# Optimization experiments

Measured on AMD Instinct MI355X. Metric: run time of the kernel, lower is better.

The kernel has to match this reference:

```python
import jax, jax.numpy as jnp
import numpy as np

NEG_SLOPE = 0.01  # torch F.leaky_relu_ default


def setup_inputs() -> dict:
    key = jax.random.key(0)
    k1, k2, k3, k4, k5 = jax.random.split(key, 5)
    N, Fin, Fout = 8192, 256, 128
    X = jax.random.normal(k1, (N, Fin), dtype=jnp.float32)
    adj = jax.random.randint(k2, (N, N), 0, 2, dtype=jnp.int32)
    W = jax.random.normal(k3, (Fout, Fin), dtype=jnp.float32) * 0.05
    b = jax.random.normal(k4, (Fout,), dtype=jnp.float32) * 0.05
    S = jax.random.normal(k5, (2 * Fout,), dtype=jnp.float32)
    return {"X": X, "adj": adj, "W": W, "b": b, "S": S}


def reference(X, adj, W, b, S):
    # X' = W X + b  -> (N, Fout)
    Xp = X @ W.T + b
    N, Fout = Xp.shape
    S_src, S_dst = S[:Fout], S[Fout:]
    # e_ij = leaky_relu(S . [x'_i ; x'_j]) = leaky_relu(S_src.x'_i + S_dst.x'_j)
    e = jax.nn.leaky_relu(
        (Xp @ S_src)[:, None] + (Xp @ S_dst)[None, :], NEG_SLOPE
    )  # (N, N)
    # neighbor set = nonzero entries of adj row plus self-loop
    mask = (adj != 0) | jnp.eye(N, dtype=bool)
    e = jnp.where(mask, e, -jnp.inf)
    attn = jax.nn.softmax(e, axis=1)  # segment softmax over each row's neighbors
    out = jax.nn.sigmoid(attn @ Xp)  # (N, Fout)
    return out
```

## Files before the change

kernel.cpp:

```cpp
#include <hip/hip_runtime.h>

typedef unsigned short u16;
typedef __attribute__((ext_vector_type(8))) u16 u16x8;
typedef __attribute__((ext_vector_type(8))) __bf16 bf16x8;
typedef __attribute__((ext_vector_type(4))) float f32x4;
typedef __attribute__((ext_vector_type(4))) int i32x4;

#define NN 8192
#define FIN 256
#define FOUT 128
#define PW 512
#define NP (NN / PW)
#define WSTRIDE 520

__device__ __forceinline__ u16 f2bf(float f) {
  unsigned u = __float_as_uint(f);
  u += 0x7fffu + ((u >> 16) & 1u);
  return (u16)(u >> 16);
}
__device__ __forceinline__ u16 f2bft(float f) {
  return (u16)(__float_as_uint(f) >> 16);
}
__device__ __forceinline__ float bf2f(u16 s) {
  return __uint_as_float(((unsigned)s) << 16);
}
__device__ __forceinline__ i32x4 ntload4(const int* p) {
  return __builtin_nontemporal_load((const i32x4*)p);
}

__global__ __launch_bounds__(256) void k_splitw(const float* __restrict__ W,
                                                u16* __restrict__ Whi,
                                                u16* __restrict__ Wlo) {
  int t = blockIdx.x * 256 + threadIdx.x;
  float w = W[t];
  u16 hi = f2bf(w);
  Whi[t] = hi;
  Wlo[t] = f2bf(w - bf2f(hi));
}

__global__ __launch_bounds__(256) void k_xp(const float* __restrict__ X,
    const u16* __restrict__ Whi, const u16* __restrict__ Wlo,
    const float* __restrict__ bias, const float* __restrict__ S,
    const int* __restrict__ adj,
    u16* __restrict__ Bsw, float* __restrict__ cexpA,
    u16* __restrict__ jebA, u16* __restrict__ jeb2A, float* __restrict__ diagW) {
  __shared__ float Xs[16 * 260];
  __shared__ float Xp[16 * 132];
  __shared__ float Ss[256];
  const int tid = threadIdx.x;
  const int i0 = blockIdx.x * 16;
  Ss[tid] = S[tid];
  {
    int r = tid >> 4, c = (tid & 15) * 16;
    const float* src = X + (size_t)(i0 + r) * FIN + c;
    float* dst = Xs + r * 260 + c;
#pragma unroll
    for (int k = 0; k < 16; k += 4) *(float4*)(dst + k) = *(const float4*)(src + k);
  }
  __syncthreads();

  const int w = tid >> 6, l = tid & 63, li = l & 15, quad = l >> 4;
  f32x4 acc[2];
  acc[0] = f32x4{0.f, 0.f, 0.f, 0.f};
  acc[1] = f32x4{0.f, 0.f, 0.f, 0.f};
  for (int k0 = 0; k0 < FIN; k0 += 32) {
    const float* xp = Xs + li * 260 + k0 + quad * 8;
    float4 xa = *(const float4*)xp;
    float4 xb = *(const float4*)(xp + 4);
    float xv[8] = {xa.x, xa.y, xa.z, xa.w, xb.x, xb.y, xb.z, xb.w};
    u16x8 ahiu, alou;
#pragma unroll
    for (int jj = 0; jj < 8; ++jj) {
      u16 h = f2bf(xv[jj]);
      ahiu[jj] = h;
      alou[jj] = f2bf(xv[jj] - bf2f(h));
    }
    bf16x8 ahi = __builtin_bit_cast(bf16x8, ahiu);
    bf16x8 alo = __builtin_bit_cast(bf16x8, alou);
#pragma unroll
    for (int t2 = 0; t2 < 2; ++t2) {
      int f = (w * 2 + t2) * 16 + li;
      size_t wofs = (size_t)f * FIN + k0 + quad * 8;
      bf16x8 bhi = __builtin_bit_cast(bf16x8, *(const u16x8*)(Whi + wofs));
      bf16x8 blo = __builtin_bit_cast(bf16x8, *(const u16x8*)(Wlo + wofs));
      acc[t2] = __builtin_amdgcn_mfma_f32_16x16x32_bf16(ahi, bhi, acc[t2], 0, 0, 0);
      acc[t2] = __builtin_amdgcn_mfma_f32_16x16x32_bf16(alo, bhi, acc[t2], 0, 0, 0);
      acc[t2] = __builtin_amdgcn_mfma_f32_16x16x32_bf16(ahi, blo, acc[t2], 0, 0, 0);
    }
  }
#pragma unroll
  for (int t2 = 0; t2 < 2; ++t2) {
    int f = (w * 2 + t2) * 16 + li;
    float bv = bias[f];
#pragma unroll
    for (int r = 0; r < 4; ++r)
      Xp[(quad * 4 + r) * 132 + f] = acc[t2][r] + bv;
  }
  __syncthreads();

  {
    int li2 = tid & 15, q2sub = (tid >> 4) & 1, nt = tid >> 5;
    int f = nt * 16 + li2;
    int rb = q2sub * 8;
    int q2 = ((i0 & 16) >> 3) + q2sub;
    u16x8 ou;
#pragma unroll
    for (int jj = 0; jj < 8; ++jj) ou[jj] = f2bf(Xp[(rb + jj) * 132 + f]);
    *(u16x8*)(Bsw + ((size_t)(i0 >> 5) * 8 + nt) * 512 + (size_t)(q2 * 16 + li2) * 8) = ou;
  }

  {
    int r = tid >> 4, sub = tid & 15;
    float pa = 0.f, pb = 0.f;
#pragma unroll
    for (int m = 0; m < 8; ++m) {
      float x = Xp[r * 132 + sub + m * 16];
      pa += x * Ss[sub + m * 16];
      pb += x * Ss[128 + sub + m * 16];
    }
    pa += __shfl_xor(pa, 1); pa += __shfl_xor(pa, 2);
    pa += __shfl_xor(pa, 4); pa += __shfl_xor(pa, 8);
    pb += __shfl_xor(pb, 1); pb += __shfl_xor(pb, 2);
    pb += __shfl_xor(pb, 4); pb += __shfl_xor(pb, 8);
    if (sub == 0) {
      int i = i0 + r;
      float cc = expf(-0.99f * pa);
      u16 ebq = f2bf(expf(pb));
      u16 e2q = f2bf(expf(0.01f * pb));
      cexpA[i] = cc;
      jebA[i] = ebq;
      jeb2A[i] = e2q;
      float wii = fmaxf(bf2f(ebq), cc * bf2f(e2q));
      float wq = bf2f(f2bft(wii));
      int ad = adj[(size_t)i * NN + i];
      diagW[i] = (ad != 0) ? 0.f : wq;
    }
  }
}

__global__ __launch_bounds__(512, 4) void k_gat(const int* __restrict__ adj,
    const u16* __restrict__ Bsw, const float* __restrict__ cexpA,
    const u16* __restrict__ jebA, const u16* __restrict__ jeb2A,
    const float* __restrict__ diagW, float* __restrict__ out) {
  __shared__ u16 wb[2][16 * WSTRIDE];
  __shared__ float sacc[16 * 132];
  __shared__ float sden[16];
  const int tid = threadIdx.x;
  const int i0 = blockIdx.x * 16;
  const int w = tid >> 6, l = tid & 63, li = l & 15, quad = l >> 4;

  {
    int r = tid >> 5, f = (tid & 31) * 4;
    int i = i0 + r;
    float dw = diagW[i];
    size_t slotbase = (size_t)(i0 >> 5) * 8;
    int laneq = ((i & 31) >> 3) * 16;
    int elem = i & 7;
    float4 v;
    float* vp = &v.x;
#pragma unroll
    for (int k = 0; k < 4; ++k) {
      int ff = f + k;
      u16 xb = Bsw[(slotbase + (ff >> 4)) * 512 + (size_t)(laneq + (ff & 15)) * 8 + elem];
      vp[k] = dw * bf2f(xb);
    }
    *(float4*)&sacc[r * 132 + f] = v;
    if (tid < 16) sden[tid] = diagW[i0 + tid];
  }

  const int r0 = 2 * w;
  const float c0 = cexpA[i0 + r0];
  const float c1 = cexpA[i0 + r0 + 1];
  const int* arow0 = adj + (size_t)(i0 + r0) * NN;
  const int* arow1 = arow0 + NN;

  i32x4 pa[4];
  ushort4 teb[2], te2[2];

  auto stage_load = [&](int p) {
    int base = p * PW + l * 4;
#pragma unroll
    for (int k = 0; k < 2; ++k) {
      pa[k * 2]     = ntload4(arow0 + base + k * 256);
      pa[k * 2 + 1] = ntload4(arow1 + base + k * 256);
      teb[k] = *(const ushort4*)(jebA + base + k * 256);
      te2[k] = *(const ushort4*)(jeb2A + base + k * 256);
    }
  };

  auto stage_store = [&](int buf) {
#pragma unroll
    for (int r2 = 0; r2 < 2; ++r2) {
      float cr = r2 ? c1 : c0;
#pragma unroll
      for (int k = 0; k < 2; ++k) {
        const i32x4 av = pa[k * 2 + r2];
        const u16* ebp = (const u16*)&teb[k];
        const u16* e2p = (const u16*)&te2[k];
        float wv[4];
#pragma unroll
        for (int e = 0; e < 4; ++e) {
          float ww = fmaxf(bf2f(ebp[e]), cr * bf2f(e2p[e]));
          wv[e] = (av[e] != 0) ? ww : 0.f;
        }
        unsigned p0 = __builtin_amdgcn_perm(__float_as_uint(wv[1]),
                                            __float_as_uint(wv[0]), 0x07060302u);
        unsigned p1 = __builtin_amdgcn_perm(__float_as_uint(wv[3]),
                                            __float_as_uint(wv[2]), 0x07060302u);
        *(uint2*)&wb[buf][(r0 + r2) * WSTRIDE + k * 256 + l * 4] = make_uint2(p0, p1);
      }
    }
  };

  f32x4 acc[8];
#pragma unroll
  for (int nt = 0; nt < 8; ++nt) acc[nt] = f32x4{0.f, 0.f, 0.f, 0.f};
  f32x4 accD = f32x4{0.f, 0.f, 0.f, 0.f};
  u16x8 onesu;
#pragma unroll
  for (int jj = 0; jj < 8; ++jj) onesu[jj] = 0x3F80;
  const bf16x8 ONES = __builtin_bit_cast(bf16x8, onesu);

  auto compute = [&](int p, int buf) {
#pragma unroll
    for (int t = 0; t < 2; ++t) {
      int s = w * 2 + t;
      u16x8 au = *(const u16x8*)&wb[buf][li * WSTRIDE + s * 32 + quad * 8];
      bf16x8 A = __builtin_bit_cast(bf16x8, au);
      const u16* bb = Bsw + (size_t)(p * 16 + s) * 4096 + (size_t)l * 8;
#pragma unroll
      for (int nt = 0; nt < 8; ++nt) {
        bf16x8 B = __builtin_bit_cast(bf16x8, *(const u16x8*)(bb + nt * 512));
        acc[nt] = __builtin_amdgcn_mfma_f32_16x16x32_bf16(A, B, acc[nt], 0, 0, 0);
      }
      accD = __builtin_amdgcn_mfma_f32_16x16x32_bf16(A, ONES, accD, 0, 0, 0);
    }
  };

  stage_load(0);
  stage_store(0);
  __syncthreads();
  for (int p = 0; p < NP; ++p) {
    if (p + 1 < NP) stage_load(p + 1);
    compute(p, p & 1);
    if (p + 1 < NP) stage_store((p + 1) & 1);
    __syncthreads();
  }

  if (li == 0) {
#pragma unroll
    for (int r = 0; r < 4; ++r) atomicAdd(&sden[quad * 4 + r], accD[r]);
  }
#pragma unroll
  for (int nt = 0; nt < 8; ++nt) {
#pragma unroll
    for (int r = 0; r < 4; ++r)
      atomicAdd(&sacc[(quad * 4 + r) * 132 + nt * 16 + li], acc[nt][r]);
  }
  __syncthreads();

  {
    int r = tid >> 5, c4 = (tid & 31) * 4;
    float4 v = *(const float4*)&sacc[r * 132 + c4];
    float rd = 1.f / sden[r];
    float o[4] = {v.x, v.y, v.z, v.w};
#pragma unroll
    for (int k = 0; k < 4; ++k) {
      float t = o[k] * rd;
      o[k] = 1.f / (1.f + __expf(-t));
    }
    *(float4*)(out + (size_t)(i0 + r) * FOUT + c4) = make_float4(o[0], o[1], o[2], o[3]);
  }
}

extern "C" void kernel_launch(void* const* d_in, const int* in_sizes, int n_in,
                              void* d_out, int out_size, void* d_ws, size_t ws_size,
                              hipStream_t stream) {
  const float* X = (const float*)d_in[0];
  const int* adj = (const int*)d_in[1];
  const float* W = (const float*)d_in[2];
  const float* bias = (const float*)d_in[3];
  const float* S = (const float*)d_in[4];
  float* out = (float*)d_out;

  char* ws = (char*)d_ws;
  u16* Bsw      = (u16*)(ws);
  u16* Whi      = (u16*)(ws + 2097152);
  u16* Wlo      = (u16*)(ws + 2162688);
  float* cexpA  = (float*)(ws + 2228224);
  u16* jebA     = (u16*)(ws + 2260992);
  u16* jeb2A    = (u16*)(ws + 2277376);
  float* diagW  = (float*)(ws + 2293760);

  hipLaunchKernelGGL(k_splitw, dim3(128), dim3(256), 0, stream, W, Whi, Wlo);
  hipLaunchKernelGGL(k_xp, dim3(512), dim3(256), 0, stream, X, Whi, Wlo, bias, S, adj,
                     Bsw, cexpA, jebA, jeb2A, diagW);
  hipLaunchKernelGGL(k_gat, dim3(512), dim3(512), 0, stream, adj, Bsw, cexpA,
                     jebA, jeb2A, diagW, out);
}
```

Baseline: 440.5 us.

## Split GAT column range across two blocks with global atomic partial sums

```diff
diff --git a/kernel.cpp b/kernel.cpp
--- a/kernel.cpp
+++ b/kernel.cpp
@@ -10,7 +10,7 @@
 #define FIN 256
 #define FOUT 128
 #define PW 512
-#define NP (NN / PW)
+#define NPB 8
 #define WSTRIDE 520
 
 __device__ __forceinline__ u16 f2bf(float f) {
@@ -23,6 +23,9 @@
 }
 __device__ __forceinline__ float bf2f(u16 s) {
   return __uint_as_float(((unsigned)s) << 16);
+}
+__device__ __forceinline__ float trunc_bf(float f) {
+  return __uint_as_float(__float_as_uint(f) & 0xffff0000u);
 }
 __device__ __forceinline__ i32x4 ntload4(const int* p) {
   return __builtin_nontemporal_load((const i32x4*)p);
@@ -43,10 +46,12 @@
     const float* __restrict__ bias, const float* __restrict__ S,
     const int* __restrict__ adj,
     u16* __restrict__ Bsw, float* __restrict__ cexpA,
-    u16* __restrict__ jebA, u16* __restrict__ jeb2A, float* __restrict__ diagW) {
+    u16* __restrict__ jebA, u16* __restrict__ jeb2A,
+    float* __restrict__ pnum, float* __restrict__ pden) {
   __shared__ float Xs[16 * 260];
   __shared__ float Xp[16 * 132];
   __shared__ float Ss[256];
+  __shared__ float ds_dw[16];
   const int tid = threadIdx.x;
   const int i0 = blockIdx.x * 16;
   Ss[tid] = S[tid];
@@ -133,40 +138,36 @@
       float wii = fmaxf(bf2f(ebq), cc * bf2f(e2q));
       float wq = bf2f(f2bft(wii));
       int ad = adj[(size_t)i * NN + i];
-      diagW[i] = (ad != 0) ? 0.f : wq;
-    }
-  }
-}
-
-__global__ __launch_bounds__(512, 4) void k_gat(const int* __restrict__ adj,
+      ds_dw[r] = (ad != 0) ? 0.f : wq;
+    }
+  }
+  __syncthreads();
+
+  {
+    int r = tid >> 4, f8 = (tid & 15) * 8;
+    int i = i0 + r;
+    float dw = ds_dw[r];
+    float o[8];
+#pragma unroll
+    for (int k = 0; k < 8; ++k)
+      o[k] = dw * bf2f(f2bf(Xp[r * 132 + f8 + k]));
+    float* np = pnum + (size_t)i * FOUT + f8;
+    *(float4*)np = make_float4(o[0], o[1], o[2], o[3]);
+    *(float4*)(np + 4) = make_float4(o[4], o[5], o[6], o[7]);
+    if ((tid & 15) == 0) pden[i] = dw;
+  }
+}
+
+__global__ __launch_bounds__(512, 8) void k_gat(const int* __restrict__ adj,
     const u16* __restrict__ Bsw, const float* __restrict__ cexpA,
     const u16* __restrict__ jebA, const u16* __restrict__ jeb2A,
-    const float* __restrict__ diagW, float* __restrict__ out) {
+    float* __restrict__ pnum, float* __restrict__ pden) {
   __shared__ u16 wb[2][16 * WSTRIDE];
-  __shared__ float sacc[16 * 132];
-  __shared__ float sden[16];
   const int tid = threadIdx.x;
-  const int i0 = blockIdx.x * 16;
+  const int rt = blockIdx.x >> 1, ch = blockIdx.x & 1;
+  const int i0 = rt * 16;
+  const int colbase = ch * 4096;
   const int w = tid >> 6, l = tid & 63, li = l & 15, quad = l >> 4;
-
-  {
-    int r = tid >> 5, f = (tid & 31) * 4;
-    int i = i0 + r;
-    float dw = diagW[i];
-    size_t slotbase = (size_t)(i0 >> 5) * 8;
-    int laneq = ((i & 31) >> 3) * 16;
-    int elem = i & 7;
-    float4 v;
-    float* vp = &v.x;
-#pragma unroll
-    for (int k = 0; k < 4; ++k) {
-      int ff = f + k;
-      u16 xb = Bsw[(slotbase + (ff >> 4)) * 512 + (size_t)(laneq + (ff & 15)) * 8 + elem];
-      vp[k] = dw * bf2f(xb);
-    }
-    *(float4*)&sacc[r * 132 + f] = v;
-    if (tid < 16) sden[tid] = diagW[i0 + tid];
-  }
 
   const int r0 = 2 * w;
   const float c0 = cexpA[i0 + r0];
@@ -176,9 +177,10 @@
 
   i32x4 pa[4];
   ushort4 teb[2], te2[2];
+  float dpart0 = 0.f, dpart1 = 0.f;
 
   auto stage_load = [&](int p) {
-    int base = p * PW + l * 4;
+    int base = colbase + p * PW + l * 4;
 #pragma unroll
     for (int k = 0; k < 2; ++k) {
       pa[k * 2]     = ntload4(arow0 + base + k * 256);
@@ -192,6 +194,7 @@
 #pragma unroll
     for (int r2 = 0; r2 < 2; ++r2) {
       float cr = r2 ? c1 : c0;
+      float dsum = 0.f;
 #pragma unroll
       for (int k = 0; k < 2; ++k) {
         const i32x4 av = pa[k * 2 + r2];
@@ -202,6 +205,7 @@
         for (int e = 0; e < 4; ++e) {
           float ww = fmaxf(bf2f(ebp[e]), cr * bf2f(e2p[e]));
           wv[e] = (av[e] != 0) ? ww : 0.f;
+          dsum += trunc_bf(wv[e]);
         }
         unsigned p0 = __builtin_amdgcn_perm(__float_as_uint(wv[1]),
                                             __float_as_uint(wv[0]), 0x07060302u);
@@ -209,17 +213,13 @@
                                             __float_as_uint(wv[2]), 0x07060302u);
         *(uint2*)&wb[buf][(r0 + r2) * WSTRIDE + k * 256 + l * 4] = make_uint2(p0, p1);
       }
+      if (r2) dpart1 += dsum; else dpart0 += dsum;
     }
   };
 
   f32x4 acc[8];
 #pragma unroll
   for (int nt = 0; nt < 8; ++nt) acc[nt] = f32x4{0.f, 0.f, 0.f, 0.f};
-  f32x4 accD = f32x4{0.f, 0.f, 0.f, 0.f};
-  u16x8 onesu;
-#pragma unroll
-  for (int jj = 0; jj < 8; ++jj) onesu[jj] = 0x3F80;
-  const bf16x8 ONES = __builtin_bit_cast(bf16x8, onesu);
 
   auto compute = [&](int p, int buf) {
 #pragma unroll
@@ -227,50 +227,57 @@
       int s = w * 2 + t;
       u16x8 au = *(const u16x8*)&wb[buf][li * WSTRIDE + s * 32 + quad * 8];
       bf16x8 A = __builtin_bit_cast(bf16x8, au);
-      const u16* bb = Bsw + (size_t)(p * 16 + s) * 4096 + (size_t)l * 8;
+      const u16* bb = Bsw + (size_t)(ch * 128 + p * 16 + s) * 4096 + (size_t)l * 8;
 #pragma unroll
       for (int nt = 0; nt < 8; ++nt) {
         bf16x8 B = __builtin_bit_cast(bf16x8, *(const u16x8*)(bb + nt * 512));
         acc[nt] = __builtin_amdgcn_mfma_f32_16x16x32_bf16(A, B, acc[nt], 0, 0, 0);
       }
-      accD = __builtin_amdgcn_mfma_f32_16x16x32_bf16(A, ONES, accD, 0, 0, 0);
     }
   };
 
   stage_load(0);
   stage_store(0);
   __syncthreads();
-  for (int p = 0; p < NP; ++p) {
-    if (p + 1 < NP) stage_load(p + 1);
+  for (int p = 0; p < NPB; ++p) {
+    if (p + 1 < NPB) stage_load(p + 1);
     compute(p, p & 1);
-    if (p + 1 < NP) stage_store((p + 1) & 1);
+    if (p + 1 < NPB) stage_store((p + 1) & 1);
     __syncthreads();
   }
 
-  if (li == 0) {
-#pragma unroll
-    for (int r = 0; r < 4; ++r) atomicAdd(&sden[quad * 4 + r], accD[r]);
-  }
+#pragma unroll
+  for (int off = 1; off < 64; off <<= 1) {
+    dpart0 += __shfl_xor(dpart0, off);
+    dpart1 += __shfl_xor(dpart1, off);
+  }
+  if (l == 0) {
+    atomicAdd(&pden[i0 + r0], dpart0);
+    atomicAdd(&pden[i0 + r0 + 1], dpart1);
+  }
+
 #pragma unroll
   for (int nt = 0; nt < 8; ++nt) {
 #pragma unroll
     for (int r = 0; r < 4; ++r)
-      atomicAdd(&sacc[(quad * 4 + r) * 132 + nt * 16 + li], acc[nt][r]);
-  }
-  __syncthreads();
-
-  {
-    int r = tid >> 5, c4 = (tid & 31) * 4;
-    float4 v = *(const float4*)&sacc[r * 132 + c4];
-    float rd = 1.f / sden[r];
-    float o[4] = {v.x, v.y, v.z, v.w};
-#pragma unroll
-    for (int k = 0; k < 4; ++k) {
-      float t = o[k] * rd;
-      o[k] = 1.f / (1.f + __expf(-t));
-    }
-    *(float4*)(out + (size_t)(i0 + r) * FOUT + c4) = make_float4(o[0], o[1], o[2], o[3]);
-  }
+      atomicAdd(&pnum[(size_t)(i0 + quad * 4 + r) * FOUT + nt * 16 + li], acc[nt][r]);
+  }
+}
+
+__global__ __launch_bounds__(256) void k_final(const float* __restrict__ pnum,
+                                               const float* __restrict__ pden,
+                                               float* __restrict__ out) {
+  int idx = blockIdx.x * 256 + threadIdx.x;
+  int row = idx >> 5, fq = (idx & 31) * 4;
+  float4 v = *(const float4*)(pnum + (size_t)row * FOUT + fq);
+  float rd = 1.f / pden[row];
+  float o[4] = {v.x, v.y, v.z, v.w};
+#pragma unroll
+  for (int k = 0; k < 4; ++k) {
+    float t = o[k] * rd;
+    o[k] = 1.f / (1.f + __expf(-t));
+  }
+  *(float4*)(out + (size_t)row * FOUT + fq) = make_float4(o[0], o[1], o[2], o[3]);
 }
 
 extern "C" void kernel_launch(void* const* d_in, const int* in_sizes, int n_in,
@@ -290,11 +297,13 @@
   float* cexpA  = (float*)(ws + 2228224);
   u16* jebA     = (u16*)(ws + 2260992);
   u16* jeb2A    = (u16*)(ws + 2277376);
-  float* diagW  = (float*)(ws + 2293760);
+  float* pnum   = (float*)(ws + 2293760);
+  float* pden   = (float*)(ws + 6488064);
 
   hipLaunchKernelGGL(k_splitw, dim3(128), dim3(256), 0, stream, W, Whi, Wlo);
   hipLaunchKernelGGL(k_xp, dim3(512), dim3(256), 0, stream, X, Whi, Wlo, bias, S, adj,
-                     Bsw, cexpA, jebA, jeb2A, diagW);
-  hipLaunchKernelGGL(k_gat, dim3(512), dim3(512), 0, stream, adj, Bsw, cexpA,
-                     jebA, jeb2A, diagW, out);
-}
+                     Bsw, cexpA, jebA, jeb2A, pnum, pden);
+  hipLaunchKernelGGL(k_gat, dim3(1024), dim3(512), 0, stream, adj, Bsw, cexpA,
+                     jebA, jeb2A, pnum, pden);
+  hipLaunchKernelGGL(k_final, dim3(1024), dim3(256), 0, stream, pnum, pden, out);
+}
```

Result: slower. 481.8 us (+9.4%).
